# Kernel optimization log

Measured on AMD Instinct MI355X. Metric: run time of the kernel, lower is better.

## Reference

```python
import jax, jax.numpy as jnp
import numpy as np

B, H, NC, CS, D = 4, 16, 64, 64, 64
BASE_LR = 1.0
EPS = 1e-6


def setup_inputs() -> dict:
    key = jax.random.key(0)
    ks = jax.random.split(key, 4)
    xk = jax.random.normal(ks[0], (B, H, NC, CS, D), jnp.float32)
    xv = jax.random.normal(ks[1], (B, H, NC, CS, D), jnp.float32)
    # weights/theta use the module's N(0, 0.02) init scale
    weight = 0.02 * jax.random.normal(ks[2], (H, D, D), jnp.float32)
    bias = jnp.zeros((H, 1, D), jnp.float32)
    gamma = jnp.ones((H, 1, D), jnp.float32)
    beta = jnp.zeros((H, 1, D), jnp.float32)
    theta = 0.02 * jax.random.normal(ks[3], (H, D, 1), jnp.float32)
    theta_bias = jnp.zeros((H, 1, 1), jnp.float32)
    alpha = jnp.zeros((CS,), jnp.float32)
    return dict(xk=xk, xv=xv, weight=weight, bias=bias, gamma=gamma,
                beta=beta, theta=theta, theta_bias=theta_bias, alpha=alpha)


def _ttt(xk, xv, weight, bias, gamma, beta, theta, theta_bias, alpha):
    Bq, Hq, NCq, CSq, Dq = xk.shape
    # TTTDynamicLearningGate: token_idx = clamp(1/arange + alpha, 0)
    token_idx = jnp.maximum(1.0 / jnp.arange(1, CSq + 1, dtype=xk.dtype) + alpha, 0.0)
    token_eta = token_idx[None, None, :, None]  # [1,1,CS,1]
    g = gamma[None]       # [1,H,1,D]
    bt = beta[None]       # [1,H,1,D]
    tb = theta_bias[None]  # [1,H,1,1]
    # detach(): tile slow weights over batch -> fast weights
    W0 = jnp.broadcast_to(weight[None], (Bq, Hq, Dq, Dq))
    b0 = jnp.broadcast_to(bias[None], (Bq, Hq, 1, Dq))

    def step(carry, chunk):
        W, b = carry
        xk_c, xv_c = chunk  # [B,H,CS,D]
        # lr gate: eta = token_eta * (base_lr * sigmoid(x @ theta + b) / head_dim)
        lr = jax.nn.sigmoid(jnp.einsum('bhkc,hcd->bhkd', xk_c, theta) + tb)
        eta = token_eta * (BASE_LR * lr / Dq)  # [B,H,CS,1]
        # forward through fast weights (depth = 1)
        z = xk_c @ W + b
        # multi-head LayerNorm, detailed
        mu = z.mean(-1, keepdims=True)
        var = ((z - mu) ** 2).mean(-1, keepdims=True)
        std = jnp.sqrt(var + EPS)
        x_hat = (z - mu) / std
        y = g * x_hat + bt
        # L2 reconstruction grad through LN (manual backward)
        grad_out = y - (xv_c - xk_c)
        gxh = grad_out * g
        grad_x = (Dq * gxh - gxh.sum(-1, keepdims=True)
                  - x_hat * (gxh * x_hat).sum(-1, keepdims=True)) / (Dq * std)
        # fast-weight delta + step()
        dW = jnp.einsum('bhkd,bhke->bhde', eta * xk_c, grad_x)
        db = (eta * grad_x).sum(-2, keepdims=True)
        Wn, bn = W - dW, b - db
        return (Wn, bn), xk_c @ Wn + bn

    chunks = (jnp.moveaxis(xk, 2, 0), jnp.moveaxis(xv, 2, 0))  # [NC,B,H,CS,D]
    (_, _), outs = jax.lax.scan(step, (W0, b0), chunks)
    return jnp.moveaxis(outs, 0, 2)  # [B,H,NC,CS,D]


def reference(xk, xv, weight, bias, gamma, beta, theta, theta_bias, alpha):
    return _ttt(xk, xv, weight, bias, gamma, beta, theta, theta_bias, alpha)
```

## Files before the change

kernel.cpp:

```cpp
#include <hip/hip_runtime.h>
#include <hip/hip_bf16.h>
#include <math.h>

#define NCC 64
#define CSC 64
#define DC 64
#define S 72
#define EPSF 1e-6f
#define LDS_BYTES 65536

typedef __attribute__((ext_vector_type(8)))  short bf16x8;
typedef __attribute__((ext_vector_type(4)))  float f32x4;
typedef __attribute__((ext_vector_type(16))) float f32x16;
typedef __attribute__((ext_vector_type(4)))  short short4v;

static __device__ __forceinline__ short cvt_bf16(float x) {
    union { __hip_bfloat16 b; short s; } u;
    u.b = __float2bfloat16(x);
    return u.s;
}

#define DPP_ROR_ADD(v, N)                                                     \
    do {                                                                      \
        union { float f; int i; } _u, _r;                                     \
        _u.f = (v);                                                           \
        _r.i = __builtin_amdgcn_mov_dpp(_u.i, 0x120 + (N), 0xF, 0xF, true);   \
        (v) += _r.f;                                                          \
    } while (0)

static __device__ __forceinline__ float red16(float v) {
    DPP_ROR_ADD(v, 1);
    DPP_ROR_ADD(v, 2);
    DPP_ROR_ADD(v, 4);
    DPP_ROR_ADD(v, 8);
    return v;
}

__global__ __launch_bounds__(512, 1) void ttt_kernel(
    const float* __restrict__ xk, const float* __restrict__ xv,
    const float* __restrict__ weight, const float* __restrict__ bias,
    const float* __restrict__ gamma, const float* __restrict__ beta,
    const float* __restrict__ theta, const float* __restrict__ theta_bias,
    const float* __restrict__ alpha, float* __restrict__ out)
{
    extern __shared__ char sb[];
    auto xs_rm = (short (*)[CSC][S])(sb);
    auto xsT   = (short (*)[DC][S]) (sb + 18432);
    auto gsT   = (short (*)[S])     (sb + 36864);
    auto Gr    = (short (*)[S])     (sb + 46080);
    auto Wtb   = (short (*)[S])     (sb + 55296);
    auto dbp   = (float (*)[DC])    (sb + 64512);

    const int t   = threadIdx.x;
    const int w   = t >> 6;
    const bool lo = (w < 4);
    const int ws  = w & 3;
    const int l   = t & 63;
    const int g   = l >> 4, la = l & 15;
    const int la5 = l & 31, hi5 = l >> 5;
    const int R   = ws >> 1, E = ws & 1;
    const int r0  = 16*ws + 4*g;
    const int ts  = 64*ws + l;
    const int bh  = blockIdx.x;
    const int h   = bh & 15;

    const size_t bh_off = (size_t)bh * NCC*CSC*DC;
    const float* xkb = xk + bh_off;
    const float* xvb = xv + bh_off;
    float*       ob  = out + bh_off;

    float gam[4], bet[4], thv[4], tok[4], bcol[4], tb = 0.f;
    float Wreg[16];
    float4 xl[4];
    float xkh[4][4], xkE[4][4], xvg[4][4], xvN[4][4];
    float bcolh = 0.f;
    f32x16 z32;

    if (lo) {
#pragma unroll
        for (int n = 0; n < 4; ++n) {
            gam[n]  = gamma[h*DC + 16*n + la];
            bet[n]  = beta [h*DC + 16*n + la];
            thv[n]  = theta[h*DC + 16*n + la];
            bcol[n] = bias [h*DC + 16*n + la];
        }
        tb = theta_bias[h];
#pragma unroll
        for (int i = 0; i < 4; ++i)
            tok[i] = fmaxf(1.0f/(float)(r0+i+1) + alpha[r0+i], 0.0f);
        const float* wg = weight + h*DC*DC;
#pragma unroll
        for (int q = 0; q < 4; ++q) {
            short4v sw;
#pragma unroll
            for (int j = 0; j < 4; ++j) {
                Wreg[4*q+j] = wg[(32*R + 8*q + 4*hi5 + j)*DC + 32*E + la5];
                sw[j] = cvt_bf16(Wreg[4*q+j]);
            }
            *(short4v*)&Wtb[32*E + la5][32*R + 8*q + 4*hi5] = sw;
        }
#pragma unroll
        for (int i4 = 0; i4 < 4; ++i4) xl[i4] = ((const float4*)xkb)[ts + 256*i4];
#pragma unroll
        for (int i = 0; i < 4; ++i)
#pragma unroll
            for (int n = 0; n < 4; ++n) {
                xkh[i][n] = xkb[(r0+i)*DC + 16*n + la];
                xvg[i][n] = xvb[(r0+i)*DC + 16*n + la];
                xkE[i][n] = xkh[i][n];
            }
#pragma unroll
        for (int i4 = 0; i4 < 4; ++i4) {
            int f = ts + 256*i4, k = f >> 4, j = f & 15;
            short4v s4;
            s4[0]=cvt_bf16(xl[i4].x); s4[1]=cvt_bf16(xl[i4].y);
            s4[2]=cvt_bf16(xl[i4].z); s4[3]=cvt_bf16(xl[i4].w);
            *(short4v*)&xs_rm[0][k][4*j] = s4;
        }
#pragma unroll
        for (int n = 0; n < 4; ++n) {
            short4v sv;
#pragma unroll
            for (int i = 0; i < 4; ++i) sv[i] = cvt_bf16(xkh[i][n]);
            *(short4v*)&xsT[0][16*n + la][r0] = sv;
        }
    } else {
        bcolh = bias[h*DC + 32*E + la5];
    }
    __syncthreads();

    for (int c = 0; c < NCC; ++c) {
        const int cb = c & 1, nb = cb ^ 1;
        const bool pf = (c + 1 < NCC);

        if (lo) {
            const bf16x8 a0 = *(const bf16x8*)&xs_rm[cb][16*ws + la][8*g];
            const bf16x8 a1 = *(const bf16x8*)&xs_rm[cb][16*ws + la][32 + 8*g];
            f32x4 zt[4];
#pragma unroll
            for (int n = 0; n < 4; ++n) {
                bf16x8 w0 = *(const bf16x8*)&Wtb[16*n + la][8*g];
                bf16x8 w1 = *(const bf16x8*)&Wtb[16*n + la][32 + 8*g];
                f32x4 zz = {0.f,0.f,0.f,0.f};
                zz = __builtin_amdgcn_mfma_f32_16x16x32_bf16(a0, w0, zz, 0,0,0);
                zz = __builtin_amdgcn_mfma_f32_16x16x32_bf16(a1, w1, zz, 0,0,0);
                zt[n] = zz;
            }
            if (pf) {
                const float* xkn = xkb + (c+1)*CSC*DC;
                const float* xvn = xvb + (c+1)*CSC*DC;
#pragma unroll
                for (int i4 = 0; i4 < 4; ++i4) xl[i4] = ((const float4*)xkn)[ts + 256*i4];
#pragma unroll
                for (int i = 0; i < 4; ++i)
#pragma unroll
                    for (int n = 0; n < 4; ++n) {
                        xkh[i][n] = xkn[(r0+i)*DC + 16*n + la];
                        xvN[i][n] = xvn[(r0+i)*DC + 16*n + la];
                    }
            }
            float gsv[4][4];
#pragma unroll
            for (int i = 0; i < 4; ++i) {
                float z0 = zt[0][i]+bcol[0], z1 = zt[1][i]+bcol[1];
                float z2 = zt[2][i]+bcol[2], z3 = zt[3][i]+bcol[3];
                float szz = red16(z0*z0 + z1*z1 + z2*z2 + z3*z3);
                float sz  = red16(z0 + z1 + z2 + z3);
                float thd = red16(xkE[i][0]*thv[0] + xkE[i][1]*thv[1] +
                                  xkE[i][2]*thv[2] + xkE[i][3]*thv[3]);
                float mu   = sz * (1.0f/DC);
                float var  = szz*(1.0f/DC) - mu*mu;
                float rstd = rsqrtf(var + EPSF);
                float ex   = __expf(-(thd + tb));
                float lr   = __builtin_amdgcn_rcpf(1.0f + ex);
                float eta  = tok[i]*lr*(1.0f/DC);
                float zz4[4] = {z0,z1,z2,z3};
                float xh[4], gxh[4], a1v = 0.f, a2v = 0.f;
#pragma unroll
                for (int n = 0; n < 4; ++n) {
                    xh[n] = (zz4[n]-mu)*rstd;
                    float y  = fmaf(gam[n], xh[n], bet[n]);
                    float go = y - xvg[i][n] + xkE[i][n];
                    gxh[n] = go*gam[n];
                    a1v += gxh[n];
                    a2v = fmaf(gxh[n], xh[n], a2v);
                }
                float s1 = red16(a1v), s2 = red16(a2v);
                float sc = rstd*(1.0f/DC)*eta;
#pragma unroll
                for (int n = 0; n < 4; ++n)
                    gsv[i][n] = (64.f*gxh[n] - s1 - xh[n]*s2)*sc;
            }
#pragma unroll
            for (int n = 0; n < 4; ++n) {
                short4v sg;
#pragma unroll
                for (int i = 0; i < 4; ++i) sg[i] = cvt_bf16(gsv[i][n]);
                *(short4v*)&gsT[16*n + la][r0] = sg;
            }
            float dbl[4];
#pragma unroll
            for (int n = 0; n < 4; ++n) {
                float dd = gsv[0][n]+gsv[1][n]+gsv[2][n]+gsv[3][n];
                dd += __shfl_xor(dd, 16);
                dd += __shfl_xor(dd, 32);
                dbl[n] = dd;
            }
            if (l < 16) {
                f32x4 dv = {dbl[0], dbl[1], dbl[2], dbl[3]};
                *(f32x4*)&dbp[ws][4*la] = dv;
            }
        } else {
            bf16x8 az[4], bz[4];
#pragma unroll
            for (int s = 0; s < 4; ++s) {
                az[s] = *(const bf16x8*)&xs_rm[cb][32*R + la5][16*s + 8*hi5];
                bz[s] = *(const bf16x8*)&Wtb[32*E + la5][16*s + 8*hi5];
            }
            f32x16 zz = {0.f,0.f,0.f,0.f,0.f,0.f,0.f,0.f,
                         0.f,0.f,0.f,0.f,0.f,0.f,0.f,0.f};
#pragma unroll
            for (int s = 0; s < 4; ++s)
                zz = __builtin_amdgcn_mfma_f32_32x32x16_bf16(az[s], bz[s], zz, 0,0,0);
            z32 = zz;
            bf16x8 bg[4];
            if (R == E) {
#pragma unroll
                for (int s = 0; s < 4; ++s) bg[s] = az[s];
            } else {
#pragma unroll
                for (int s = 0; s < 4; ++s)
                    bg[s] = *(const bf16x8*)&xs_rm[cb][32*E + la5][16*s + 8*hi5];
            }
            f32x16 gg = {0.f,0.f,0.f,0.f,0.f,0.f,0.f,0.f,
                         0.f,0.f,0.f,0.f,0.f,0.f,0.f,0.f};
#pragma unroll
            for (int s = 0; s < 4; ++s)
                gg = __builtin_amdgcn_mfma_f32_32x32x16_bf16(az[s], bg[s], gg, 0,0,0);
#pragma unroll
            for (int q = 0; q < 4; ++q) {
                short4v sg;
#pragma unroll
                for (int j = 0; j < 4; ++j) sg[j] = cvt_bf16(gg[4*q+j] + 1.0f);
                *(short4v*)&Gr[32*E + la5][32*R + 8*q + 4*hi5] = sg;
            }
        }
        __syncthreads();

        if (lo) {
            bf16x8 ax[4], bx[4];
#pragma unroll
            for (int s = 0; s < 4; ++s) {
                ax[s] = *(const bf16x8*)&xsT[cb][32*R + la5][16*s + 8*hi5];
                bx[s] = *(const bf16x8*)&gsT[32*E + la5][16*s + 8*hi5];
            }
            f32x16 dw = {0.f,0.f,0.f,0.f,0.f,0.f,0.f,0.f,
                         0.f,0.f,0.f,0.f,0.f,0.f,0.f,0.f};
#pragma unroll
            for (int s = 0; s < 4; ++s)
                dw = __builtin_amdgcn_mfma_f32_32x32x16_bf16(ax[s], bx[s], dw, 0,0,0);
#pragma unroll
            for (int q = 0; q < 4; ++q) {
                short4v sw;
#pragma unroll
                for (int j = 0; j < 4; ++j) {
                    Wreg[4*q+j] -= dw[4*q+j];
                    sw[j] = cvt_bf16(Wreg[4*q+j]);
                }
                *(short4v*)&Wtb[32*E + la5][32*R + 8*q + 4*hi5] = sw;
            }
            if (pf) {
#pragma unroll
                for (int i4 = 0; i4 < 4; ++i4) {
                    int f = ts + 256*i4, k = f >> 4, j = f & 15;
                    short4v s4;
                    s4[0]=cvt_bf16(xl[i4].x); s4[1]=cvt_bf16(xl[i4].y);
                    s4[2]=cvt_bf16(xl[i4].z); s4[3]=cvt_bf16(xl[i4].w);
                    *(short4v*)&xs_rm[nb][k][4*j] = s4;
                }
#pragma unroll
                for (int n = 0; n < 4; ++n) {
                    short4v sv;
#pragma unroll
                    for (int i = 0; i < 4; ++i) sv[i] = cvt_bf16(xkh[i][n]);
                    *(short4v*)&xsT[nb][16*n + la][r0] = sv;
                }
#pragma unroll
                for (int i = 0; i < 4; ++i)
#pragma unroll
                    for (int n = 0; n < 4; ++n) {
                        xkE[i][n] = xkh[i][n];
                        xvg[i][n] = xvN[i][n];
                    }
            }
            {
                f32x4 s = *(const f32x4*)&dbp[0][4*la];
#pragma unroll
                for (int p = 1; p < 4; ++p) {
                    f32x4 d = *(const f32x4*)&dbp[p][4*la];
#pragma unroll
                    for (int n = 0; n < 4; ++n) s[n] += d[n];
                }
#pragma unroll
                for (int n = 0; n < 4; ++n) bcol[n] -= s[n];
            }
        } else {
            bf16x8 ag[4], bq[4];
#pragma unroll
            for (int s = 0; s < 4; ++s) {
                ag[s] = *(const bf16x8*)&Gr[32*R + la5][16*s + 8*hi5];
                bq[s] = *(const bf16x8*)&gsT[32*E + la5][16*s + 8*hi5];
            }
            f32x16 og = {0.f,0.f,0.f,0.f,0.f,0.f,0.f,0.f,
                         0.f,0.f,0.f,0.f,0.f,0.f,0.f,0.f};
#pragma unroll
            for (int s = 0; s < 4; ++s)
                og = __builtin_amdgcn_mfma_f32_32x32x16_bf16(ag[s], bq[s], og, 0,0,0);
            float* oc = ob + c*CSC*DC;
#pragma unroll
            for (int q = 0; q < 4; ++q)
#pragma unroll
                for (int j = 0; j < 4; ++j) {
                    int r = 4*q + j;
                    oc[(32*R + 8*q + 4*hi5 + j)*DC + 32*E + la5] =
                        z32[r] - og[r] + bcolh;
                }
            {
                int idx = 4*(la5 & 15) + 2*E + (la5 >> 4);
                float s0 = dbp[0][idx];
                s0 += dbp[1][idx];
                s0 += dbp[2][idx];
                s0 += dbp[3][idx];
                bcolh -= s0;
            }
        }
        __syncthreads();
    }
}

extern "C" void kernel_launch(void* const* d_in, const int* in_sizes, int n_in,
                              void* d_out, int out_size, void* d_ws, size_t ws_size,
                              hipStream_t stream) {
    const float* xk         = (const float*)d_in[0];
    const float* xv         = (const float*)d_in[1];
    const float* weight     = (const float*)d_in[2];
    const float* bias       = (const float*)d_in[3];
    const float* gamma      = (const float*)d_in[4];
    const float* beta       = (const float*)d_in[5];
    const float* theta      = (const float*)d_in[6];
    const float* theta_bias = (const float*)d_in[7];
    const float* alpha      = (const float*)d_in[8];
    float* out = (float*)d_out;

    (void)hipFuncSetAttribute((const void*)ttt_kernel,
                              hipFuncAttributeMaxDynamicSharedMemorySize,
                              LDS_BYTES);
    ttt_kernel<<<64, 512, LDS_BYTES, stream>>>(xk, xv, weight, bias, gamma, beta,
                                               theta, theta_bias, alpha, out);
}
```

Before: 157.7 us.

## Pipeline fast-weight update off critical path using stale-weight forward plus correction

```diff
diff --git a/kernel.cpp b/kernel.cpp
--- a/kernel.cpp
+++ b/kernel.cpp
@@ -6,18 +6,24 @@
 #define CSC 64
 #define DC 64
 #define S 72
+#define SZ 68
 #define EPSF 1e-6f
-#define LDS_BYTES 65536
+#define LDS_BYTES 120832
 
 typedef __attribute__((ext_vector_type(8)))  short bf16x8;
 typedef __attribute__((ext_vector_type(4)))  float f32x4;
 typedef __attribute__((ext_vector_type(16))) float f32x16;
 typedef __attribute__((ext_vector_type(4)))  short short4v;
+typedef __attribute__((ext_vector_type(8)))  short short8v;
 
 static __device__ __forceinline__ short cvt_bf16(float x) {
     union { __hip_bfloat16 b; short s; } u;
     u.b = __float2bfloat16(x);
     return u.s;
+}
+static __device__ __forceinline__ float bf16_to_f(unsigned short hw) {
+    union { unsigned u; float f; } v; v.u = ((unsigned)hw) << 16;
+    return v.f;
 }
 
 #define DPP_ROR_ADD(v, N)                                                     \
@@ -35,6 +41,9 @@
     DPP_ROR_ADD(v, 8);
     return v;
 }
+
+#define MFMA16 __builtin_amdgcn_mfma_f32_16x16x32_bf16
+#define MFMA32 __builtin_amdgcn_mfma_f32_32x32x16_bf16
 
 __global__ __launch_bounds__(512, 1) void ttt_kernel(
     const float* __restrict__ xk, const float* __restrict__ xv,
@@ -46,76 +55,81 @@
     extern __shared__ char sb[];
     auto xs_rm = (short (*)[CSC][S])(sb);
     auto xsT   = (short (*)[DC][S]) (sb + 18432);
-    auto gsT   = (short (*)[S])     (sb + 36864);
-    auto Gr    = (short (*)[S])     (sb + 46080);
-    auto Wtb   = (short (*)[S])     (sb + 55296);
-    auto dbp   = (float (*)[DC])    (sb + 64512);
-
-    const int t   = threadIdx.x;
-    const int w   = t >> 6;
-    const bool lo = (w < 4);
-    const int ws  = w & 3;
-    const int l   = t & 63;
-    const int g   = l >> 4, la = l & 15;
-    const int la5 = l & 31, hi5 = l >> 5;
-    const int R   = ws >> 1, E = ws & 1;
-    const int r0  = 16*ws + 4*g;
-    const int ts  = 64*ws + l;
-    const int bh  = blockIdx.x;
-    const int h   = bh & 15;
+    auto gsT   = (short (*)[DC][S]) (sb + 46080);
+    auto Gr    = (short (*)[DC][S]) (sb + 64512);
+    auto Cx    = (short (*)[S])     (sb + 82944);
+    auto Wtb   = (short (*)[S])     (sb + 92160);
+    auto zpb   = (float (*)[SZ])    (sb + 101376);
+    auto dbp   = (float (*)[4][DC]) (sb + 118784);
+
+    const int t    = threadIdx.x;
+    const int w    = t >> 6;
+    const bool crit = (w < 4);
+    const int ws   = w & 3;
+    const int l    = t & 63;
+    const int g    = l >> 4, la = l & 15;
+    const int la5  = l & 31, h5 = l >> 5;
+    const int R    = ws >> 1, E = ws & 1;
+    const int r0   = 16*ws + 4*g;
+    const int ts   = 64*ws + l;
+    const int bh   = blockIdx.x;
+    const int h    = bh & 15;
 
     const size_t bh_off = (size_t)bh * NCC*CSC*DC;
     const float* xkb = xk + bh_off;
     const float* xvb = xv + bh_off;
     float*       ob  = out + bh_off;
 
-    float gam[4], bet[4], thv[4], tok[4], bcol[4], tb = 0.f;
+    float gam[4], bet[4], thv[4], tok[4], tb = 0.f;
+    float xvg[4][4], xvN[4][4];
     float Wreg[16];
+    float bcolh = 0.f;
     float4 xl[4];
-    float xkh[4][4], xkE[4][4], xvg[4][4], xvN[4][4];
-    float bcolh = 0.f;
-    f32x16 z32;
-
-    if (lo) {
+    float xkh[4][4];
+
+    if (crit) {
 #pragma unroll
         for (int n = 0; n < 4; ++n) {
-            gam[n]  = gamma[h*DC + 16*n + la];
-            bet[n]  = beta [h*DC + 16*n + la];
-            thv[n]  = theta[h*DC + 16*n + la];
-            bcol[n] = bias [h*DC + 16*n + la];
+            gam[n] = gamma[h*DC + 16*n + la];
+            bet[n] = beta [h*DC + 16*n + la];
+            thv[n] = theta[h*DC + 16*n + la];
         }
         tb = theta_bias[h];
 #pragma unroll
         for (int i = 0; i < 4; ++i)
             tok[i] = fmaxf(1.0f/(float)(r0+i+1) + alpha[r0+i], 0.0f);
+#pragma unroll
+        for (int i = 0; i < 4; ++i)
+#pragma unroll
+            for (int n = 0; n < 4; ++n)
+                xvg[i][n] = xvb[(r0+i)*DC + 16*n + la];
+    } else {
+#pragma unroll
+        for (int j = 0; j < 4; ++j) xl[j] = ((const float4*)xkb)[ts + 256*j];
+#pragma unroll
+        for (int i = 0; i < 4; ++i)
+#pragma unroll
+            for (int n = 0; n < 4; ++n)
+                xkh[i][n] = xkb[(r0+i)*DC + 16*n + la];
+        bcolh = bias[h*DC + 32*E + la5];
         const float* wg = weight + h*DC*DC;
 #pragma unroll
         for (int q = 0; q < 4; ++q) {
             short4v sw;
 #pragma unroll
             for (int j = 0; j < 4; ++j) {
-                Wreg[4*q+j] = wg[(32*R + 8*q + 4*hi5 + j)*DC + 32*E + la5];
+                Wreg[4*q+j] = wg[(32*R + 8*q + 4*h5 + j)*DC + 32*E + la5];
                 sw[j] = cvt_bf16(Wreg[4*q+j]);
             }
-            *(short4v*)&Wtb[32*E + la5][32*R + 8*q + 4*hi5] = sw;
-        }
-#pragma unroll
-        for (int i4 = 0; i4 < 4; ++i4) xl[i4] = ((const float4*)xkb)[ts + 256*i4];
-#pragma unroll
-        for (int i = 0; i < 4; ++i)
-#pragma unroll
-            for (int n = 0; n < 4; ++n) {
-                xkh[i][n] = xkb[(r0+i)*DC + 16*n + la];
-                xvg[i][n] = xvb[(r0+i)*DC + 16*n + la];
-                xkE[i][n] = xkh[i][n];
-            }
-#pragma unroll
-        for (int i4 = 0; i4 < 4; ++i4) {
-            int f = ts + 256*i4, k = f >> 4, j = f & 15;
+            *(short4v*)&Wtb[32*E + la5][32*R + 8*q + 4*h5] = sw;
+        }
+#pragma unroll
+        for (int j4 = 0; j4 < 4; ++j4) {
+            int f = ts + 256*j4, k = f >> 4, jj = f & 15;
             short4v s4;
-            s4[0]=cvt_bf16(xl[i4].x); s4[1]=cvt_bf16(xl[i4].y);
-            s4[2]=cvt_bf16(xl[i4].z); s4[3]=cvt_bf16(xl[i4].w);
-            *(short4v*)&xs_rm[0][k][4*j] = s4;
+            s4[0]=cvt_bf16(xl[j4].x); s4[1]=cvt_bf16(xl[j4].y);
+            s4[2]=cvt_bf16(xl[j4].z); s4[3]=cvt_bf16(xl[j4].w);
+            *(short4v*)&xs_rm[0][k][4*jj] = s4;
         }
 #pragma unroll
         for (int n = 0; n < 4; ++n) {
@@ -124,46 +138,87 @@
             for (int i = 0; i < 4; ++i) sv[i] = cvt_bf16(xkh[i][n]);
             *(short4v*)&xsT[0][16*n + la][r0] = sv;
         }
-    } else {
-        bcolh = bias[h*DC + 32*E + la5];
+    }
+    if (t < 64) {
+        short8v z8 = {0,0,0,0,0,0,0,0};
+#pragma unroll
+        for (int j = 0; j < 9; ++j) {
+            *(short8v*)&Cx[t][8*j]        = z8;
+            *(short8v*)&gsT[1][t][8*j]    = z8;
+        }
     }
     __syncthreads();
 
+    if (!crit) {
+        bf16x8 az0[4], bz0[4];
+#pragma unroll
+        for (int s = 0; s < 4; ++s) {
+            az0[s] = *(const bf16x8*)&xs_rm[0][32*R + la5][16*s + 8*h5];
+            bz0[s] = *(const bf16x8*)&Wtb[32*E + la5][16*s + 8*h5];
+        }
+        f32x16 zz = {0.f,0.f,0.f,0.f,0.f,0.f,0.f,0.f,
+                     0.f,0.f,0.f,0.f,0.f,0.f,0.f,0.f};
+#pragma unroll
+        for (int s = 0; s < 4; ++s) zz = MFMA32(az0[s], bz0[s], zz, 0,0,0);
+#pragma unroll
+        for (int q = 0; q < 4; ++q) {
+            f32x4 zv;
+#pragma unroll
+            for (int j = 0; j < 4; ++j) zv[j] = zz[4*q+j] + bcolh;
+            *(f32x4*)&zpb[32*E + la5][32*R + 8*q + 4*h5] = zv;
+        }
+        const float* xk1 = xkb + CSC*DC;
+#pragma unroll
+        for (int j = 0; j < 4; ++j) xl[j] = ((const float4*)xk1)[ts + 256*j];
+#pragma unroll
+        for (int i = 0; i < 4; ++i)
+#pragma unroll
+            for (int n = 0; n < 4; ++n)
+                xkh[i][n] = xk1[(r0+i)*DC + 16*n + la];
+    }
+    __syncthreads();
+
     for (int c = 0; c < NCC; ++c) {
         const int cb = c & 1, nb = cb ^ 1;
-        const bool pf = (c + 1 < NCC);
-
-        if (lo) {
-            const bf16x8 a0 = *(const bf16x8*)&xs_rm[cb][16*ws + la][8*g];
-            const bf16x8 a1 = *(const bf16x8*)&xs_rm[cb][16*ws + la][32 + 8*g];
-            f32x4 zt[4];
+        const int cp3 = c % 3, cn3 = (c+1) % 3, co3 = (c+2) % 3;
+        const bool pf1 = (c + 1 < NCC), pf2 = (c + 2 < NCC);
+
+        f32x4 zt[4];
+        bf16x8 az[4];
+
+        if (crit) {
+            if (pf1) {
+                const float* xvn = xvb + (c+1)*CSC*DC;
+#pragma unroll
+                for (int i = 0; i < 4; ++i)
+#pragma unroll
+                    for (int n = 0; n < 4; ++n)
+                        xvN[i][n] = xvn[(r0+i)*DC + 16*n + la];
+            }
+#pragma unroll
+            for (int n = 0; n < 4; ++n)
+                zt[n] = *(const f32x4*)&zpb[16*n + la][r0];
+            const bf16x8 cx0 = *(const bf16x8*)&Cx[16*ws + la][8*g];
+            const bf16x8 cx1 = *(const bf16x8*)&Cx[16*ws + la][32 + 8*g];
 #pragma unroll
             for (int n = 0; n < 4; ++n) {
-                bf16x8 w0 = *(const bf16x8*)&Wtb[16*n + la][8*g];
-                bf16x8 w1 = *(const bf16x8*)&Wtb[16*n + la][32 + 8*g];
-                f32x4 zz = {0.f,0.f,0.f,0.f};
-                zz = __builtin_amdgcn_mfma_f32_16x16x32_bf16(a0, w0, zz, 0,0,0);
-                zz = __builtin_amdgcn_mfma_f32_16x16x32_bf16(a1, w1, zz, 0,0,0);
-                zt[n] = zz;
-            }
-            if (pf) {
-                const float* xkn = xkb + (c+1)*CSC*DC;
-                const float* xvn = xvb + (c+1)*CSC*DC;
-#pragma unroll
-                for (int i4 = 0; i4 < 4; ++i4) xl[i4] = ((const float4*)xkn)[ts + 256*i4];
+                bf16x8 q0 = *(const bf16x8*)&gsT[nb][16*n + la][8*g];
+                bf16x8 q1 = *(const bf16x8*)&gsT[nb][16*n + la][32 + 8*g];
+                zt[n] = MFMA16(cx0, q0, zt[n], 0,0,0);
+                zt[n] = MFMA16(cx1, q1, zt[n], 0,0,0);
+            }
+            float xkE[4][4];
+#pragma unroll
+            for (int n = 0; n < 4; ++n) {
+                short4v pk = *(const short4v*)&xsT[cp3][16*n + la][r0];
 #pragma unroll
                 for (int i = 0; i < 4; ++i)
-#pragma unroll
-                    for (int n = 0; n < 4; ++n) {
-                        xkh[i][n] = xkn[(r0+i)*DC + 16*n + la];
-                        xvN[i][n] = xvn[(r0+i)*DC + 16*n + la];
-                    }
+                    xkE[i][n] = bf16_to_f((unsigned short)pk[i]);
             }
             float gsv[4][4];
 #pragma unroll
             for (int i = 0; i < 4; ++i) {
-                float z0 = zt[0][i]+bcol[0], z1 = zt[1][i]+bcol[1];
-                float z2 = zt[2][i]+bcol[2], z3 = zt[3][i]+bcol[3];
+                float z0 = zt[0][i], z1 = zt[1][i], z2 = zt[2][i], z3 = zt[3][i];
                 float szz = red16(z0*z0 + z1*z1 + z2*z2 + z3*z3);
                 float sz  = red16(z0 + z1 + z2 + z3);
                 float thd = red16(xkE[i][0]*thv[0] + xkE[i][1]*thv[1] +
@@ -196,7 +251,7 @@
                 short4v sg;
 #pragma unroll
                 for (int i = 0; i < 4; ++i) sg[i] = cvt_bf16(gsv[i][n]);
-                *(short4v*)&gsT[16*n + la][r0] = sg;
+                *(short4v*)&gsT[cb][16*n + la][r0] = sg;
             }
             float dbl[4];
 #pragma unroll
@@ -208,21 +263,37 @@
             }
             if (l < 16) {
                 f32x4 dv = {dbl[0], dbl[1], dbl[2], dbl[3]};
-                *(f32x4*)&dbp[ws][4*la] = dv;
+                *(f32x4*)&dbp[cb][ws][4*la] = dv;
             }
         } else {
-            bf16x8 az[4], bz[4];
-#pragma unroll
-            for (int s = 0; s < 4; ++s) {
-                az[s] = *(const bf16x8*)&xs_rm[cb][32*R + la5][16*s + 8*hi5];
-                bz[s] = *(const bf16x8*)&Wtb[32*E + la5][16*s + 8*hi5];
-            }
-            f32x16 zz = {0.f,0.f,0.f,0.f,0.f,0.f,0.f,0.f,
-                         0.f,0.f,0.f,0.f,0.f,0.f,0.f,0.f};
+            if (c > 0) {
+                bf16x8 ax[4], bx[4];
+#pragma unroll
+                for (int s = 0; s < 4; ++s) {
+                    ax[s] = *(const bf16x8*)&xsT[co3][32*R + la5][16*s + 8*h5];
+                    bx[s] = *(const bf16x8*)&gsT[nb][32*E + la5][16*s + 8*h5];
+                }
+                f32x16 dw = {0.f,0.f,0.f,0.f,0.f,0.f,0.f,0.f,
+                             0.f,0.f,0.f,0.f,0.f,0.f,0.f,0.f};
+#pragma unroll
+                for (int s = 0; s < 4; ++s) dw = MFMA32(ax[s], bx[s], dw, 0,0,0);
+#pragma unroll
+                for (int q = 0; q < 4; ++q) {
+                    short4v sw;
+#pragma unroll
+                    for (int j = 0; j < 4; ++j) {
+                        Wreg[4*q+j] -= dw[4*q+j];
+                        sw[j] = cvt_bf16(Wreg[4*q+j]);
+                    }
+                    *(short4v*)&Wtb[32*E + la5][32*R + 8*q + 4*h5] = sw;
+                }
+                int idx = 4*(la5 & 15) + 2*E + (la5 >> 4);
+                bcolh -= dbp[nb][0][idx] + dbp[nb][1][idx] +
+                         dbp[nb][2][idx] + dbp[nb][3][idx];
+            }
 #pragma unroll
             for (int s = 0; s < 4; ++s)
-                zz = __builtin_amdgcn_mfma_f32_32x32x16_bf16(az[s], bz[s], zz, 0,0,0);
-            z32 = zz;
+                az[s] = *(const bf16x8*)&xs_rm[cb][32*R + la5][16*s + 8*h5];
             bf16x8 bg[4];
             if (R == E) {
 #pragma unroll
@@ -230,108 +301,105 @@
             } else {
 #pragma unroll
                 for (int s = 0; s < 4; ++s)
-                    bg[s] = *(const bf16x8*)&xs_rm[cb][32*E + la5][16*s + 8*hi5];
+                    bg[s] = *(const bf16x8*)&xs_rm[cb][32*E + la5][16*s + 8*h5];
             }
             f32x16 gg = {0.f,0.f,0.f,0.f,0.f,0.f,0.f,0.f,
                          0.f,0.f,0.f,0.f,0.f,0.f,0.f,0.f};
 #pragma unroll
-            for (int s = 0; s < 4; ++s)
-                gg = __builtin_amdgcn_mfma_f32_32x32x16_bf16(az[s], bg[s], gg, 0,0,0);
+            for (int s = 0; s < 4; ++s) gg = MFMA32(az[s], bg[s], gg, 0,0,0);
 #pragma unroll
             for (int q = 0; q < 4; ++q) {
                 short4v sg;
 #pragma unroll
-                for (int j = 0; j < 4; ++j) sg[j] = cvt_bf16(gg[4*q+j] + 1.0f);
-                *(short4v*)&Gr[32*E + la5][32*R + 8*q + 4*hi5] = sg;
-            }
-        }
-        __syncthreads();
-
-        if (lo) {
-            bf16x8 ax[4], bx[4];
-#pragma unroll
-            for (int s = 0; s < 4; ++s) {
-                ax[s] = *(const bf16x8*)&xsT[cb][32*R + la5][16*s + 8*hi5];
-                bx[s] = *(const bf16x8*)&gsT[32*E + la5][16*s + 8*hi5];
-            }
-            f32x16 dw = {0.f,0.f,0.f,0.f,0.f,0.f,0.f,0.f,
-                         0.f,0.f,0.f,0.f,0.f,0.f,0.f,0.f};
-#pragma unroll
-            for (int s = 0; s < 4; ++s)
-                dw = __builtin_amdgcn_mfma_f32_32x32x16_bf16(ax[s], bx[s], dw, 0,0,0);
-#pragma unroll
-            for (int q = 0; q < 4; ++q) {
-                short4v sw;
-#pragma unroll
-                for (int j = 0; j < 4; ++j) {
-                    Wreg[4*q+j] -= dw[4*q+j];
-                    sw[j] = cvt_bf16(Wreg[4*q+j]);
-                }
-                *(short4v*)&Wtb[32*E + la5][32*R + 8*q + 4*hi5] = sw;
-            }
-            if (pf) {
-#pragma unroll
-                for (int i4 = 0; i4 < 4; ++i4) {
-                    int f = ts + 256*i4, k = f >> 4, j = f & 15;
+                for (int j = 0; j < 4; ++j) sg[j] = cvt_bf16(-(gg[4*q+j] + 1.0f));
+                *(short4v*)&Gr[cb][32*E + la5][32*R + 8*q + 4*h5] = sg;
+            }
+            if (pf1) {
+#pragma unroll
+                for (int j4 = 0; j4 < 4; ++j4) {
+                    int f = ts + 256*j4, k = f >> 4, jj = f & 15;
                     short4v s4;
-                    s4[0]=cvt_bf16(xl[i4].x); s4[1]=cvt_bf16(xl[i4].y);
-                    s4[2]=cvt_bf16(xl[i4].z); s4[3]=cvt_bf16(xl[i4].w);
-                    *(short4v*)&xs_rm[nb][k][4*j] = s4;
+                    s4[0]=cvt_bf16(xl[j4].x); s4[1]=cvt_bf16(xl[j4].y);
+                    s4[2]=cvt_bf16(xl[j4].z); s4[3]=cvt_bf16(xl[j4].w);
+                    *(short4v*)&xs_rm[nb][k][4*jj] = s4;
                 }
 #pragma unroll
                 for (int n = 0; n < 4; ++n) {
                     short4v sv;
 #pragma unroll
                     for (int i = 0; i < 4; ++i) sv[i] = cvt_bf16(xkh[i][n]);
-                    *(short4v*)&xsT[nb][16*n + la][r0] = sv;
-                }
+                    *(short4v*)&xsT[cn3][16*n + la][r0] = sv;
+                }
+            }
+        }
+        __syncthreads();
+
+        if (crit) {
+            const bf16x8 ag0 = *(const bf16x8*)&Gr[cb][16*ws + la][8*g];
+            const bf16x8 ag1 = *(const bf16x8*)&Gr[cb][16*ws + la][32 + 8*g];
+            float* oc = ob + c*CSC*DC;
+#pragma unroll
+            for (int n = 0; n < 4; ++n) {
+                bf16x8 q0 = *(const bf16x8*)&gsT[cb][16*n + la][8*g];
+                bf16x8 q1 = *(const bf16x8*)&gsT[cb][16*n + la][32 + 8*g];
+                f32x4 og = zt[n];
+                og = MFMA16(ag0, q0, og, 0,0,0);
+                og = MFMA16(ag1, q1, og, 0,0,0);
 #pragma unroll
                 for (int i = 0; i < 4; ++i)
-#pragma unroll
-                    for (int n = 0; n < 4; ++n) {
-                        xkE[i][n] = xkh[i][n];
+                    oc[(r0+i)*DC + 16*n + la] = og[i];
+            }
+            if (pf1) {
+#pragma unroll
+                for (int i = 0; i < 4; ++i)
+#pragma unroll
+                    for (int n = 0; n < 4; ++n)
                         xvg[i][n] = xvN[i][n];
-                    }
-            }
-            {
-                f32x4 s = *(const f32x4*)&dbp[0][4*la];
-#pragma unroll
-                for (int p = 1; p < 4; ++p) {
-                    f32x4 d = *(const f32x4*)&dbp[p][4*la];
-#pragma unroll
-                    for (int n = 0; n < 4; ++n) s[n] += d[n];
-                }
-#pragma unroll
-                for (int n = 0; n < 4; ++n) bcol[n] -= s[n];
             }
         } else {
-            bf16x8 ag[4], bq[4];
-#pragma unroll
-            for (int s = 0; s < 4; ++s) {
-                ag[s] = *(const bf16x8*)&Gr[32*R + la5][16*s + 8*hi5];
-                bq[s] = *(const bf16x8*)&gsT[32*E + la5][16*s + 8*hi5];
-            }
-            f32x16 og = {0.f,0.f,0.f,0.f,0.f,0.f,0.f,0.f,
-                         0.f,0.f,0.f,0.f,0.f,0.f,0.f,0.f};
-#pragma unroll
-            for (int s = 0; s < 4; ++s)
-                og = __builtin_amdgcn_mfma_f32_32x32x16_bf16(ag[s], bq[s], og, 0,0,0);
-            float* oc = ob + c*CSC*DC;
-#pragma unroll
-            for (int q = 0; q < 4; ++q)
-#pragma unroll
-                for (int j = 0; j < 4; ++j) {
-                    int r = 4*q + j;
-                    oc[(32*R + 8*q + 4*hi5 + j)*DC + 32*E + la5] =
-                        z32[r] - og[r] + bcolh;
-                }
-            {
-                int idx = 4*(la5 & 15) + 2*E + (la5 >> 4);
-                float s0 = dbp[0][idx];
-                s0 += dbp[1][idx];
-                s0 += dbp[2][idx];
-                s0 += dbp[3][idx];
-                bcolh -= s0;
+            if (pf2) {
+                const float* xk2 = xkb + (c+2)*CSC*DC;
+#pragma unroll
+                for (int j = 0; j < 4; ++j) xl[j] = ((const float4*)xk2)[ts + 256*j];
+#pragma unroll
+                for (int i = 0; i < 4; ++i)
+#pragma unroll
+                    for (int n = 0; n < 4; ++n)
+                        xkh[i][n] = xk2[(r0+i)*DC + 16*n + la];
+            }
+            if (pf1) {
+                bf16x8 an[4], bw[4];
+#pragma unroll
+                for (int s = 0; s < 4; ++s) {
+                    an[s] = *(const bf16x8*)&xs_rm[nb][32*R + la5][16*s + 8*h5];
+                    bw[s] = *(const bf16x8*)&Wtb[32*E + la5][16*s + 8*h5];
+                }
+                f32x16 zz = {0.f,0.f,0.f,0.f,0.f,0.f,0.f,0.f,
+                             0.f,0.f,0.f,0.f,0.f,0.f,0.f,0.f};
+#pragma unroll
+                for (int s = 0; s < 4; ++s) zz = MFMA32(an[s], bw[s], zz, 0,0,0);
+#pragma unroll
+                for (int q = 0; q < 4; ++q) {
+                    f32x4 zv;
+#pragma unroll
+                    for (int j = 0; j < 4; ++j) zv[j] = zz[4*q+j] + bcolh;
+                    *(f32x4*)&zpb[32*E + la5][32*R + 8*q + 4*h5] = zv;
+                }
+                bf16x8 bn[4];
+#pragma unroll
+                for (int s = 0; s < 4; ++s)
+                    bn[s] = *(const bf16x8*)&xs_rm[nb][32*E + la5][16*s + 8*h5];
+                f32x16 xx = {0.f,0.f,0.f,0.f,0.f,0.f,0.f,0.f,
+                             0.f,0.f,0.f,0.f,0.f,0.f,0.f,0.f};
+#pragma unroll
+                for (int s = 0; s < 4; ++s) xx = MFMA32(az[s], bn[s], xx, 0,0,0);
+#pragma unroll
+                for (int q = 0; q < 4; ++q) {
+                    short4v sx;
+#pragma unroll
+                    for (int j = 0; j < 4; ++j) sx[j] = cvt_bf16(-(xx[4*q+j] + 1.0f));
+                    *(short4v*)&Cx[32*E + la5][32*R + 8*q + 4*h5] = sx;
+                }
             }
         }
         __syncthreads();
```

Result: slower. 178.6 us (+13.3%).
